# Kernel optimization log

Hardware: AMD Instinct MI355X
Metric: run time of the kernel (lower is better)

## Reference

```python
import jax, jax.numpy as jnp
import numpy as np

B, P, C = 128, 8732, 21          # batch, num_priors (SSD300), num_classes incl. background
TOP_K = 200
VAR0, VAR1 = 0.1, 0.2            # SSD prior variances
CONF_THRESH = 0.01
NMS_THRESH = 0.45


def setup_inputs() -> dict:
    key = jax.random.key(0)
    k1, k2, k3, k4 = jax.random.split(key, 4)
    loc_data = jax.random.normal(k1, (B, P, 4), jnp.float32)
    conf_data = jax.random.normal(k2, (B * P, C), jnp.float32)
    # priors: (cx, cy, w, h) in [0,1], positive widths/heights
    cxy = jax.random.uniform(k3, (P, 2), jnp.float32)
    wh = jax.random.uniform(k4, (P, 2), jnp.float32, minval=0.02, maxval=0.3)
    prior_data = jnp.concatenate([cxy, wh], axis=-1)
    return {"loc_data": loc_data, "conf_data": conf_data, "prior_data": prior_data}


def _decode(loc, priors):
    # loc: [B,P,4], priors: [P,4] (cx,cy,w,h) -> corner boxes [B,P,4]
    xy = priors[:, :2] + loc[..., :2] * VAR0 * priors[:, 2:]
    wh = priors[:, 2:] * jnp.exp(loc[..., 2:] * VAR1)
    return jnp.concatenate([xy - wh * 0.5, xy + wh * 0.5], axis=-1)


def _nms_single(boxes, scores, idxs):
    # boxes [P,4] corners, scores [P] (-1 where below conf_thresh), idxs [P] int class ids
    x1, y1, x2, y2 = boxes[:, 0], boxes[:, 1], boxes[:, 2], boxes[:, 3]
    areas = (x2 - x1) * (y2 - y1)

    def body(s, _):
        i = jnp.argmax(s)          # highest remaining score
        si = s[i]
        valid = si > 0.0
        bi = boxes[i]
        # IoU of bi against all boxes
        ix1 = jnp.maximum(bi[0], x1)
        iy1 = jnp.maximum(bi[1], y1)
        ix2 = jnp.minimum(bi[2], x2)
        iy2 = jnp.minimum(bi[3], y2)
        inter = jnp.maximum(ix2 - ix1, 0.0) * jnp.maximum(iy2 - iy1, 0.0)
        area_i = (bi[2] - bi[0]) * (bi[3] - bi[1])
        iou = inter / (area_i + areas - inter)
        # class-aware (batched) NMS: only suppress same-class boxes; also kills i itself (iou=1)
        suppress = (iou > NMS_THRESH) & (idxs == idxs[i])
        s_new = jnp.where(suppress, -1.0, s)
        row = jnp.where(
            valid,
            jnp.concatenate([bi, si[None], idxs[i].astype(jnp.float32)[None]]),
            jnp.zeros(6, dtype=boxes.dtype),
        )
        return s_new, row

    _, rows = jax.lax.scan(body, scores, None, length=TOP_K)
    return rows  # [TOP_K, 6] = (x1,y1,x2,y2,score,class)


def reference(loc_data, conf_data, prior_data):
    # softmax over classes, drop background, per-prior best fg class
    conf = jax.nn.softmax(conf_data, axis=-1)[:, 1:].reshape(B, P, C - 1)
    scores = conf.max(axis=-1)           # [B,P]
    cls = jnp.argmax(conf, axis=-1)      # [B,P] fg class id (0..C-2)
    boxes = _decode(loc_data, prior_data)  # [B,P,4]
    masked = jnp.where(scores > CONF_THRESH, scores, -1.0)
    return jax.vmap(_nms_single)(boxes, masked, cls)  # [B, TOP_K, 6]
```

## Files before the change

### kernel.cpp

```cpp
#include <hip/hip_runtime.h>


typedef unsigned long long u64;

#define BATCH 128
#define NPRIOR 8732
#define NCLS 21
#define TOPK 200
#define T 1024
#define TARGET 256
#define CAP 384
#define NBIN 4096
#define KW 6
#define NCHUNK 9

__device__ __forceinline__ double exp_fast(double x) {
  const double LOG2E = 1.4426950408889634;
  const double LN2_HI = 6.93147180369123816490e-01;
  const double LN2_LO = 1.90821492927058770002e-10;
  double n = rint(x * LOG2E);
  double r = fma(-n, LN2_HI, x);
  r = fma(-n, LN2_LO, r);
  double p = 2.505210838544172e-08;
  p = fma(p, r, 2.755731922398589e-07);
  p = fma(p, r, 2.7557319223985893e-06);
  p = fma(p, r, 2.48015873015873e-05);
  p = fma(p, r, 1.984126984126984e-04);
  p = fma(p, r, 1.388888888888889e-03);
  p = fma(p, r, 8.333333333333333e-03);
  p = fma(p, r, 4.1666666666666664e-02);
  p = fma(p, r, 1.6666666666666666e-01);
  p = fma(p, r, 0.5);
  p = fma(p, r, 1.0);
  p = fma(p, r, 1.0);
  double scale = __longlong_as_double(((long long)(1023 + (int)n)) << 52);
  return p * scale;
}

__global__ __launch_bounds__(256) void prep_kernel(
    const float* __restrict__ conf, u64* __restrict__ keys) {
  const int r = blockIdx.x * 256 + threadIdx.x;
  const float* __restrict__ rp = conf + (long long)r * NCLS;
  float cr[NCLS];
#pragma unroll
  for (int j = 0; j < NCLS; ++j) cr[j] = rp[j];
  float m = cr[0];
#pragma unroll
  for (int j = 1; j < NCLS; ++j) m = fmaxf(m, cr[j]);
  float sum = __expf(cr[0] - m);
  float bestr = cr[1];
  float beste = __expf(cr[1] - m);
  sum += beste;
  int bi = 1;
#pragma unroll
  for (int j = 2; j < NCLS; ++j) {
    float rv = cr[j];
    float ej = __expf(rv - m);
    sum += ej;
    if (rv > bestr) { bestr = rv; bi = j; beste = ej; }
  }
  float score = __fdividef(beste, sum);

  const int p = r % NPRIOR;
  u64 key = 0ULL;
  if (score > 0.01f) {
    key = ((u64)__float_as_uint(score) << 32) |
          ((u64)(16383 - p) << 10) | (u64)(bi - 1);
  }
  keys[r] = key;
}

__device__ __forceinline__ void radix_cut(const int* hist, int tid, int tcap,
                                          int* wtot, int* cut) {
  if (tid == 0) cut[2] = 0;
  const int base = tid * 4;
  const int cs = hist[base] + hist[base + 1] + hist[base + 2] + hist[base + 3];
  const int lane = tid & 63;
  int suf = cs;
#pragma unroll
  for (int off = 1; off < 64; off <<= 1) {
    int v = __shfl_down(suf, off);
    if (lane + off < 64) suf += v;
  }
  if (lane == 0) wtot[tid >> 6] = suf;
  __syncthreads();
  if (tid < 16) {
    int v = wtot[tid];
    int s = v;
#pragma unroll
    for (int off = 1; off < 16; off <<= 1) {
      int o = __shfl_down(s, off);
      if (tid + off < 16) s += o;
    }
    if (tid == 0) wtot[16] = s;
    wtot[tid] = s - v;
  }
  __syncthreads();
  const int total = wtot[16];
  if (total > 0) {
    const int target = total < tcap ? total : tcap;
    const int S = suf + wtot[tid >> 6];
    const int Snext = S - cs;
    if (S >= target && Snext < target) {
      int acc = Snext;
      for (int bn = base + 3; bn >= base; --bn) {
        acc += hist[bn];
        if (acc >= target) {
          cut[0] = bn; cut[1] = acc - hist[bn]; cut[2] = acc;
          break;
        }
      }
    }
  }
  __syncthreads();
}

__global__ __launch_bounds__(T) void selnms_kernel(
    const float* __restrict__ loc, const float* __restrict__ conf,
    const float* __restrict__ prior, const u64* __restrict__ keys,
    float* __restrict__ out) {
  __shared__ int hist[NBIN];
  __shared__ u64 buf[CAP];
  __shared__ u64 ebuf[CAP];
  __shared__ u64 buf2[CAP];
  __shared__ float4 cbox[CAP];
  __shared__ float car[CAP];
  __shared__ int ccl[CAP];
  __shared__ u64 KILL[CAP * KW];
  __shared__ int wtot[17];
  __shared__ int cut1[3], cut2[3];
  __shared__ u64 Ash[KW], KFsh[KW], ACCsh[KW];
  __shared__ float4 abox[TOPK];
  __shared__ float aar[TOPK];
  __shared__ int acl[TOPK];
  __shared__ int sh_cnt, sh_nA;

  const int tid = threadIdx.x;
  const int b = blockIdx.x;
  const float* confb = conf + (long long)b * (NPRIOR * NCLS);
  const float4* loc4 = ((const float4*)loc) + (long long)b * NPRIOR;
  const float4* pr4 = (const float4*)prior;
  float* outb = out + (long long)b * (TOPK * 6);
  const u64* kb = keys + (long long)b * NPRIOR;

  u64 kreg[NCHUNK];
#pragma unroll
  for (int c = 0; c < NCHUNK; ++c) {
    const int i = c * T + tid;
    kreg[c] = (i < NPRIOR) ? kb[i] : 0ULL;
  }
  if (tid == 0) sh_nA = 0;

  u64 ub = ~0ULL;
  int Mr = 0, total = 0;
  while (true) {
    for (int i = tid; i < NBIN; i += T) hist[i] = 0;
    __syncthreads();
#pragma unroll
    for (int c = 0; c < NCHUNK; ++c) {
      u64 k = kreg[c];
      if (k && k < ub) atomicAdd(&hist[(int)((k >> 46) & 0xFFF)], 1);
    }
    __syncthreads();
    radix_cut(hist, tid, TARGET, wtot, cut1);
    total = wtot[16];
    int M = cut1[2];
    if (M == 0) break;
    const int c1 = cut1[0];
    const int baseA = cut1[1];
    const bool need2 = (M > CAP);
    int c2 = 0;
    if (need2) {
      for (int i = tid; i < NBIN; i += T) hist[i] = 0;
      __syncthreads();
#pragma unroll
      for (int c = 0; c < NCHUNK; ++c) {
        u64 k = kreg[c];
        if (k && k < ub && (int)((k >> 46) & 0xFFF) == c1)
          atomicAdd(&hist[(int)((k >> 34) & 0xFFF)], 1);
      }
      __syncthreads();
      const int tcap2 = (total < TARGET ? total : TARGET) - baseA;
      radix_cut(hist, tid, tcap2, wtot, cut2);
      c2 = cut2[0];
      M = baseA + cut2[2];
      if (M > CAP) {
        int Md = M - hist[c2];
        if (Md > 0) { M = Md; c2 = c2 + 1; } else { M = CAP; }
      }
    }
    if (tid == 0) sh_cnt = 0;
    const u64 ubold = ub;
    ub = need2 ? (((u64)c1 << 46) + ((u64)c2 << 34)) : ((u64)c1 << 46);
    __syncthreads();
#pragma unroll
    for (int c = 0; c < NCHUNK; ++c) {
      u64 k = kreg[c];
      bool psel = false;
      if (k && k < ubold) {
        int b1 = (int)((k >> 46) & 0xFFF);
        psel = need2 ? (b1 > c1 || (b1 == c1 && (int)((k >> 34) & 0xFFF) >= c2))
                     : (b1 >= c1);
      }
      u64 mask = __ballot(psel ? 1 : 0);
      if (mask) {
        int lane = tid & 63;
        int leader = __ffsll((unsigned long long)mask) - 1;
        int bpos = 0;
        if (lane == leader) bpos = atomicAdd(&sh_cnt, __popcll(mask));
        bpos = __shfl(bpos, leader);
        if (psel) {
          int pos = bpos + __popcll(mask & ((1ULL << lane) - 1ULL));
          if (pos < CAP) buf[pos] = k;
        }
      }
    }
    __syncthreads();
    Mr = sh_cnt;
    if (Mr > CAP) Mr = CAP;
    if (Mr == 0) break;

    float4 lreg = make_float4(0.f, 0.f, 0.f, 0.f);
    float4 preg = make_float4(0.f, 0.f, 0.f, 0.f);
    int myp = 0, mycl = 0;
    if (tid < Mr) {
      u64 ak = buf[tid];
      mycl = (int)(ak & 0x1FULL);
      myp = 16383 - (int)((ak >> 10) & 0x3FFFULL);
      lreg = loc4[myp];
      preg = pr4[myp];
      const float* crow = confb + (long long)myp * NCLS;
      float cr[NCLS];
#pragma unroll
      for (int j = 0; j < NCLS; ++j) cr[j] = crow[j];
      double m = (double)cr[0];
#pragma unroll
      for (int j = 1; j < NCLS; ++j) m = fmax(m, (double)cr[j]);
      double sum = 0.0, best = -1.0;
#pragma unroll
      for (int j = 0; j < NCLS; ++j) {
        double ej = exp_fast((double)cr[j] - m);
        sum += ej;
        if (j >= 1 && ej > best) best = ej;
      }
      double score = best / sum;
      u64 sb = (u64)__double_as_longlong(score);
      ebuf[tid] = ((sb >> 24) << 24) | ((u64)(16383 - myp) << 10) | (u64)mycl;
    }
    if (tid < KW) { Ash[tid] = 0ULL; KFsh[tid] = 0ULL; }
    __syncthreads();
    const int nA0 = sh_nA;

    if (tid < Mr) {
      u64 ka = ebuf[tid];
      int ra = 0;
      int i = 0;
      for (; i + 8 <= Mr; i += 8) {
        u64 k0 = ebuf[i], k1 = ebuf[i + 1], k2 = ebuf[i + 2], k3 = ebuf[i + 3];
        u64 k4 = ebuf[i + 4], k5 = ebuf[i + 5], k6 = ebuf[i + 6],
            k7 = ebuf[i + 7];
        ra += (int)(k0 > ka) + (int)(k1 > ka) + (int)(k2 > ka) +
              (int)(k3 > ka) + (int)(k4 > ka) + (int)(k5 > ka) +
              (int)(k6 > ka) + (int)(k7 > ka);
      }
      for (; i < Mr; ++i) ra += (int)(ebuf[i] > ka);
      buf2[ra] = ka;
      double cx = (double)preg.x + (double)lreg.x * 0.1 * (double)preg.z;
      double cy = (double)preg.y + (double)lreg.y * 0.1 * (double)preg.w;
      double w = (double)preg.z * exp_fast((double)lreg.z * 0.2);
      double h = (double)preg.w * exp_fast((double)lreg.w * 0.2);
      float x1 = (float)(cx - w * 0.5), y1 = (float)(cy - h * 0.5);
      float x2 = (float)(cx + w * 0.5), y2 = (float)(cy + h * 0.5);
      cbox[ra] = make_float4(x1, y1, x2, y2);
      car[ra] = (x2 - x1) * (y2 - y1);
      ccl[ra] = mycl;
    }
    __syncthreads();

    if (nA0 > 0 && tid < Mr) {
      const int t = tid;
      float4 my = cbox[t];
      float mar = car[t];
      int mcl = ccl[t];
      bool sup = false;
      for (int a = 0; a < nA0; ++a) {
        if (acl[a] == mcl) {
          float4 ab = abox[a];
          float ix1 = fmaxf(ab.x, my.x), iy1 = fmaxf(ab.y, my.y);
          float ix2 = fminf(ab.z, my.z), iy2 = fminf(ab.w, my.w);
          float inter = fmaxf(ix2 - ix1, 0.f) * fmaxf(iy2 - iy1, 0.f);
          if (inter > 0.45f * (aar[a] + mar - inter)) sup = true;
        }
      }
      if (sup) atomicOr(&Ash[t >> 6], 1ULL << (t & 63));
    }
    for (int idx = tid; idx < KW * 512; idx += T) {
      const int seg = idx >> 9;
      const int t = idx & 511;
      if (t < Mr) {
        const int i0 = seg * 64;
        int i1 = i0 + 64;
        if (i1 > Mr) i1 = Mr;
        u64 mm = 0ULL;
        if (i1 > t) {
          float4 my = cbox[t];
          float mar = car[t];
          int mcl = ccl[t];
          int is = (i0 > t + 1) ? i0 : (t + 1);
#pragma unroll 4
          for (int i = is; i < i1; ++i) {
            if (ccl[i] == mcl) {
              float4 cb = cbox[i];
              float ix1 = fmaxf(my.x, cb.x), iy1 = fmaxf(my.y, cb.y);
              float ix2 = fminf(my.z, cb.z), iy2 = fminf(my.w, cb.w);
              float inter = fmaxf(ix2 - ix1, 0.f) * fmaxf(iy2 - iy1, 0.f);
              if (inter > 0.45f * (mar + car[i] - inter))
                mm |= 1ULL << (i - i0);
            }
          }
        }
        KILL[t * KW + seg] = mm;
        if (mm) atomicOr(&KFsh[t >> 6], 1ULL << (t & 63));
      }
    }
    __syncthreads();
    if (tid < 64) {
      u64 A0, A1, A2, A3, A4, A5;
      {
        u64 v[KW];
#pragma unroll
        for (int w = 0; w < KW; ++w) {
          int rem = Mr - 64 * w;
          u64 vm =
              (rem >= 64) ? ~0ULL : (rem <= 0 ? 0ULL : ((1ULL << rem) - 1ULL));
          v[w] = vm & ~Ash[w];
        }
        A0 = v[0]; A1 = v[1]; A2 = v[2]; A3 = v[3]; A4 = v[4]; A5 = v[5];
      }
      u64 C0 = 0, C1 = 0, C2 = 0, C3 = 0, C4 = 0, C5 = 0;
      int nacc = nA0;
      bool full = false;
#define KILLUPD(cidx) do { const u64* kc = &KILL[(cidx) * KW];      \
      A0 &= ~kc[0]; A1 &= ~kc[1]; A2 &= ~kc[2];                     \
      A3 &= ~kc[3]; A4 &= ~kc[4]; A5 &= ~kc[5]; } while (0)
#define RESW(w, Aw, Cw) if (!full) {                                \
      const u64 KFw = KFsh[w];                                      \
      int lim = Mr - (w) * 64; if (lim > 64) lim = 64;              \
      for (int q = 0; q < lim; ++q) {                               \
        if ((Aw >> q) & 1ULL) {                                     \
          Cw |= 1ULL << q; ++nacc;                                  \
          if (nacc == TOPK) { full = true; break; }                 \
          if ((KFw >> q) & 1ULL) KILLUPD((w) * 64 + q);             \
        } } }
      RESW(0, A0, C0)
      RESW(1, A1, C1)
      RESW(2, A2, C2)
      RESW(3, A3, C3)
      RESW(4, A4, C4)
      RESW(5, A5, C5)
#undef RESW
#undef KILLUPD
      if (tid == 0) {
        ACCsh[0] = C0; ACCsh[1] = C1; ACCsh[2] = C2;
        ACCsh[3] = C3; ACCsh[4] = C4; ACCsh[5] = C5;
        sh_nA = nacc;
      }
    }
    __syncthreads();
    if (tid < Mr) {
      const int t = tid;
      const int w = t >> 6, q = t & 63;
      const u64 accw = ACCsh[w];
      if ((accw >> q) & 1ULL) {
        int rank = nA0;
#pragma unroll
        for (int w2 = 0; w2 < KW; ++w2)
          if (w2 < w) rank += __popcll(ACCsh[w2]);
        rank += __popcll(accw & ((q == 0) ? 0ULL : ((1ULL << q) - 1ULL)));
        float4 bx = cbox[t];
        float sc =
            (float)__longlong_as_double((long long)((buf2[t] >> 24) << 24));
        float* o = outb + rank * 6;
        o[0] = bx.x; o[1] = bx.y; o[2] = bx.z; o[3] = bx.w;
        o[4] = sc; o[5] = (float)ccl[t];
        abox[rank] = bx; aar[rank] = car[t]; acl[rank] = ccl[t];
      }
    }
    __syncthreads();
    if (sh_nA >= TOPK) break;
    if (total - Mr <= 0) break;
  }
  __syncthreads();
  const int nAf = sh_nA;
  for (int i = nAf * 6 + tid; i < TOPK * 6; i += T) outb[i] = 0.0f;
}

extern "C" void kernel_launch(void* const* d_in, const int* in_sizes, int n_in,
                              void* d_out, int out_size, void* d_ws,
                              size_t ws_size, hipStream_t stream) {
  const float* loc = (const float*)d_in[0];
  const float* conf = (const float*)d_in[1];
  const float* prior = (const float*)d_in[2];
  float* out = (float*)d_out;

  u64* keys = (u64*)d_ws;
  const int nrows_blocks = (BATCH * NPRIOR) / 256;

  prep_kernel<<<nrows_blocks, 256, 0, stream>>>(conf, keys);
  selnms_kernel<<<BATCH, T, 0, stream>>>(loc, conf, prior, keys, out);
}
```

Measured before the change: 204.9 us.

## Fuse softmax key prep into NMS kernel and rebuild kill mask via ballots

The separate prep kernel that computes softmax scores and packed sort keys is removed. Each block of the detection kernel now computes its own batch's keys in registers, which avoids the round trip of keys through global workspace and one kernel launch. The pairwise suppression matrix is also restructured: six waves each own a column segment and build KILL rows with wave ballots, reading classes from a packed byte array. The cost is that the whole conf read (about 94 MB, with strided per-thread rows) now runs on only 128 blocks instead of thousands, and the mask build uses fewer threads.

```diff
diff --git a/kernel.cpp b/kernel.cpp
--- a/kernel.cpp
+++ b/kernel.cpp
@@ -37,39 +37,6 @@
   return p * scale;
 }
 
-__global__ __launch_bounds__(256) void prep_kernel(
-    const float* __restrict__ conf, u64* __restrict__ keys) {
-  const int r = blockIdx.x * 256 + threadIdx.x;
-  const float* __restrict__ rp = conf + (long long)r * NCLS;
-  float cr[NCLS];
-#pragma unroll
-  for (int j = 0; j < NCLS; ++j) cr[j] = rp[j];
-  float m = cr[0];
-#pragma unroll
-  for (int j = 1; j < NCLS; ++j) m = fmaxf(m, cr[j]);
-  float sum = __expf(cr[0] - m);
-  float bestr = cr[1];
-  float beste = __expf(cr[1] - m);
-  sum += beste;
-  int bi = 1;
-#pragma unroll
-  for (int j = 2; j < NCLS; ++j) {
-    float rv = cr[j];
-    float ej = __expf(rv - m);
-    sum += ej;
-    if (rv > bestr) { bestr = rv; bi = j; beste = ej; }
-  }
-  float score = __fdividef(beste, sum);
-
-  const int p = r % NPRIOR;
-  u64 key = 0ULL;
-  if (score > 0.01f) {
-    key = ((u64)__float_as_uint(score) << 32) |
-          ((u64)(16383 - p) << 10) | (u64)(bi - 1);
-  }
-  keys[r] = key;
-}
-
 __device__ __forceinline__ void radix_cut(const int* hist, int tid, int tcap,
                                           int* wtot, int* cut) {
   if (tid == 0) cut[2] = 0;
@@ -115,10 +82,9 @@
   __syncthreads();
 }
 
-__global__ __launch_bounds__(T) void selnms_kernel(
+__global__ __launch_bounds__(T) void detect_kernel(
     const float* __restrict__ loc, const float* __restrict__ conf,
-    const float* __restrict__ prior, const u64* __restrict__ keys,
-    float* __restrict__ out) {
+    const float* __restrict__ prior, float* __restrict__ out) {
   __shared__ int hist[NBIN];
   __shared__ u64 buf[CAP];
   __shared__ u64 ebuf[CAP];
@@ -126,6 +92,7 @@
   __shared__ float4 cbox[CAP];
   __shared__ float car[CAP];
   __shared__ int ccl[CAP];
+  __shared__ __align__(4) unsigned char cclb[CAP];
   __shared__ u64 KILL[CAP * KW];
   __shared__ int wtot[17];
   __shared__ int cut1[3], cut2[3];
@@ -141,13 +108,39 @@
   const float4* loc4 = ((const float4*)loc) + (long long)b * NPRIOR;
   const float4* pr4 = (const float4*)prior;
   float* outb = out + (long long)b * (TOPK * 6);
-  const u64* kb = keys + (long long)b * NPRIOR;
 
   u64 kreg[NCHUNK];
 #pragma unroll
   for (int c = 0; c < NCHUNK; ++c) {
-    const int i = c * T + tid;
-    kreg[c] = (i < NPRIOR) ? kb[i] : 0ULL;
+    const int r = c * T + tid;
+    u64 key = 0ULL;
+    if (r < NPRIOR) {
+      const float* __restrict__ rp = confb + (long long)r * NCLS;
+      float cr[NCLS];
+#pragma unroll
+      for (int j = 0; j < NCLS; ++j) cr[j] = rp[j];
+      float m = cr[0];
+#pragma unroll
+      for (int j = 1; j < NCLS; ++j) m = fmaxf(m, cr[j]);
+      float sum = __expf(cr[0] - m);
+      float bestr = cr[1];
+      float beste = __expf(cr[1] - m);
+      sum += beste;
+      int bi = 1;
+#pragma unroll
+      for (int j = 2; j < NCLS; ++j) {
+        float rv = cr[j];
+        float ej = __expf(rv - m);
+        sum += ej;
+        if (rv > bestr) { bestr = rv; bi = j; beste = ej; }
+      }
+      float score = __fdividef(beste, sum);
+      if (score > 0.01f) {
+        key = ((u64)__float_as_uint(score) << 32) |
+              ((u64)(16383 - r) << 10) | (u64)(bi - 1);
+      }
+    }
+    kreg[c] = key;
   }
   if (tid == 0) sh_nA = 0;
 
@@ -274,6 +267,7 @@
       cbox[ra] = make_float4(x1, y1, x2, y2);
       car[ra] = (x2 - x1) * (y2 - y1);
       ccl[ra] = mycl;
+      cclb[ra] = (unsigned char)mycl;
     }
     __syncthreads();
 
@@ -294,33 +288,39 @@
       }
       if (sup) atomicOr(&Ash[t >> 6], 1ULL << (t & 63));
     }
-    for (int idx = tid; idx < KW * 512; idx += T) {
-      const int seg = idx >> 9;
-      const int t = idx & 511;
-      if (t < Mr) {
-        const int i0 = seg * 64;
-        int i1 = i0 + 64;
-        if (i1 > Mr) i1 = Mr;
-        u64 mm = 0ULL;
-        if (i1 > t) {
-          float4 my = cbox[t];
-          float mar = car[t];
-          int mcl = ccl[t];
-          int is = (i0 > t + 1) ? i0 : (t + 1);
-#pragma unroll 4
-          for (int i = is; i < i1; ++i) {
-            if (ccl[i] == mcl) {
-              float4 cb = cbox[i];
-              float ix1 = fmaxf(my.x, cb.x), iy1 = fmaxf(my.y, cb.y);
-              float ix2 = fminf(my.z, cb.z), iy2 = fminf(my.w, cb.w);
+    {
+      const int wv = tid >> 6;
+      const int lane = tid & 63;
+      if (wv < KW) {
+        const int s = wv;
+        const int j = s * 64 + lane;
+        float4 ob = make_float4(0.f, 0.f, 0.f, 0.f);
+        float oar = 0.f;
+        int ocl = -1;
+        if (j < Mr) { ob = cbox[j]; oar = car[j]; ocl = ccl[j]; }
+        for (int t0 = 0; t0 < Mr; t0 += 64) {
+          u64 myrow = 0ULL;
+          const int tend = (t0 + 64 < Mr) ? (t0 + 64) : Mr;
+          unsigned cw = 0;
+          for (int t = t0; t < tend; ++t) {
+            if ((t & 3) == 0) cw = *(const unsigned*)&cclb[t & ~3];
+            const int clt = (int)((cw >> ((t & 3) * 8)) & 0xFF);
+            float4 tb = cbox[t];
+            bool kill = false;
+            if (j > t && j < Mr && clt == ocl) {
+              float tar = (tb.z - tb.x) * (tb.w - tb.y);
+              float ix1 = fmaxf(tb.x, ob.x), iy1 = fmaxf(tb.y, ob.y);
+              float ix2 = fminf(tb.z, ob.z), iy2 = fminf(tb.w, ob.w);
               float inter = fmaxf(ix2 - ix1, 0.f) * fmaxf(iy2 - iy1, 0.f);
-              if (inter > 0.45f * (mar + car[i] - inter))
-                mm |= 1ULL << (i - i0);
+              kill = inter > 0.45f * (tar + oar - inter);
             }
+            u64 mm = __ballot(kill ? 1 : 0);
+            if (lane == (t - t0)) myrow = mm;
           }
+          if (t0 + lane < Mr) KILL[(t0 + lane) * KW + s] = myrow;
+          u64 kf = __ballot(myrow != 0ULL);
+          if (lane == 0 && kf) atomicOr(&KFsh[t0 >> 6], kf);
         }
-        KILL[t * KW + seg] = mm;
-        if (mm) atomicOr(&KFsh[t >> 6], 1ULL << (t & 63));
       }
     }
     __syncthreads();
@@ -402,10 +402,7 @@
   const float* conf = (const float*)d_in[1];
   const float* prior = (const float*)d_in[2];
   float* out = (float*)d_out;
-
-  u64* keys = (u64*)d_ws;
-  const int nrows_blocks = (BATCH * NPRIOR) / 256;
-
-  prep_kernel<<<nrows_blocks, 256, 0, stream>>>(conf, keys);
-  selnms_kernel<<<BATCH, T, 0, stream>>>(loc, conf, prior, keys, out);
+  (void)d_ws; (void)ws_size;
+
+  detect_kernel<<<BATCH, T, 0, stream>>>(loc, conf, prior, out);
 }
```

New measurement: 233.1 us. 13.8% more time.

## Stage keys in LDS and iterate only same-class candidates via class bitmasks

Applied to the files above, without the earlier changes.

Per-class 64-bit membership masks over the sorted candidate list are built with shared atomics. The pairwise kill-mask loop then walks only the set bits of same-class candidates instead of scanning every candidate and branching on class. Separately, the per-thread register copy of the keys is replaced by a 70KB shared-memory array that the histogram and selection passes re-read. This cuts IoU work and register pressure, but adds shared traffic and LDS use that may limit occupancy, which matters little with one block per batch.

```diff
diff --git a/kernel.cpp b/kernel.cpp
--- a/kernel.cpp
+++ b/kernel.cpp
@@ -12,7 +12,7 @@
 #define CAP 384
 #define NBIN 4096
 #define KW 6
-#define NCHUNK 9
+#define NCLM 20
 
 __device__ __forceinline__ double exp_fast(double x) {
   const double LOG2E = 1.4426950408889634;
@@ -119,6 +119,7 @@
     const float* __restrict__ loc, const float* __restrict__ conf,
     const float* __restrict__ prior, const u64* __restrict__ keys,
     float* __restrict__ out) {
+  __shared__ u64 Ks[NPRIOR];
   __shared__ int hist[NBIN];
   __shared__ u64 buf[CAP];
   __shared__ u64 ebuf[CAP];
@@ -127,6 +128,7 @@
   __shared__ float car[CAP];
   __shared__ int ccl[CAP];
   __shared__ u64 KILL[CAP * KW];
+  __shared__ u64 CLSM[NCLM][KW];
   __shared__ int wtot[17];
   __shared__ int cut1[3], cut2[3];
   __shared__ u64 Ash[KW], KFsh[KW], ACCsh[KW];
@@ -143,22 +145,17 @@
   float* outb = out + (long long)b * (TOPK * 6);
   const u64* kb = keys + (long long)b * NPRIOR;
 
-  u64 kreg[NCHUNK];
-#pragma unroll
-  for (int c = 0; c < NCHUNK; ++c) {
-    const int i = c * T + tid;
-    kreg[c] = (i < NPRIOR) ? kb[i] : 0ULL;
-  }
+  for (int i = tid; i < NPRIOR; i += T) Ks[i] = kb[i];
   if (tid == 0) sh_nA = 0;
+  __syncthreads();
 
   u64 ub = ~0ULL;
   int Mr = 0, total = 0;
   while (true) {
     for (int i = tid; i < NBIN; i += T) hist[i] = 0;
     __syncthreads();
-#pragma unroll
-    for (int c = 0; c < NCHUNK; ++c) {
-      u64 k = kreg[c];
+    for (int i = tid; i < NPRIOR; i += T) {
+      u64 k = Ks[i];
       if (k && k < ub) atomicAdd(&hist[(int)((k >> 46) & 0xFFF)], 1);
     }
     __syncthreads();
@@ -173,9 +170,8 @@
     if (need2) {
       for (int i = tid; i < NBIN; i += T) hist[i] = 0;
       __syncthreads();
-#pragma unroll
-      for (int c = 0; c < NCHUNK; ++c) {
-        u64 k = kreg[c];
+      for (int i = tid; i < NPRIOR; i += T) {
+        u64 k = Ks[i];
         if (k && k < ub && (int)((k >> 46) & 0xFFF) == c1)
           atomicAdd(&hist[(int)((k >> 34) & 0xFFF)], 1);
       }
@@ -193,9 +189,8 @@
     const u64 ubold = ub;
     ub = need2 ? (((u64)c1 << 46) + ((u64)c2 << 34)) : ((u64)c1 << 46);
     __syncthreads();
-#pragma unroll
-    for (int c = 0; c < NCHUNK; ++c) {
-      u64 k = kreg[c];
+    for (int i = tid; i < NPRIOR; i += T) {
+      u64 k = Ks[i];
       bool psel = false;
       if (k && k < ubold) {
         int b1 = (int)((k >> 46) & 0xFFF);
@@ -248,6 +243,7 @@
       ebuf[tid] = ((sb >> 24) << 24) | ((u64)(16383 - myp) << 10) | (u64)mycl;
     }
     if (tid < KW) { Ash[tid] = 0ULL; KFsh[tid] = 0ULL; }
+    if (tid < NCLM * KW) ((u64*)CLSM)[tid] = 0ULL;
     __syncthreads();
     const int nA0 = sh_nA;
 
@@ -274,6 +270,7 @@
       cbox[ra] = make_float4(x1, y1, x2, y2);
       car[ra] = (x2 - x1) * (y2 - y1);
       ccl[ra] = mycl;
+      atomicOr(&CLSM[mycl][ra >> 6], 1ULL << (ra & 63));
     }
     __syncthreads();
 
@@ -299,25 +296,25 @@
       const int t = idx & 511;
       if (t < Mr) {
         const int i0 = seg * 64;
-        int i1 = i0 + 64;
-        if (i1 > Mr) i1 = Mr;
         u64 mm = 0ULL;
-        if (i1 > t) {
-          float4 my = cbox[t];
-          float mar = car[t];
-          int mcl = ccl[t];
-          int is = (i0 > t + 1) ? i0 : (t + 1);
-#pragma unroll 4
-          for (int i = is; i < i1; ++i) {
-            if (ccl[i] == mcl) {
-              float4 cb = cbox[i];
-              float ix1 = fmaxf(my.x, cb.x), iy1 = fmaxf(my.y, cb.y);
-              float ix2 = fminf(my.z, cb.z), iy2 = fminf(my.w, cb.w);
-              float inter = fmaxf(ix2 - ix1, 0.f) * fmaxf(iy2 - iy1, 0.f);
-              if (inter > 0.45f * (mar + car[i] - inter))
-                mm |= 1ULL << (i - i0);
-            }
-          }
+        u64 cm = CLSM[ccl[t]][seg];
+        const int d = t - i0;
+        if (d >= 63) cm = 0ULL;
+        else if (d >= 0) cm &= ~((1ULL << (d + 1)) - 1ULL);
+        if (cm) {
+          const float4 my = cbox[t];
+          const float mar = (my.z - my.x) * (my.w - my.y);
+          do {
+            const int l = __ffsll((unsigned long long)cm) - 1;
+            cm &= cm - 1ULL;
+            const int i = i0 + l;
+            const float4 cb = cbox[i];
+            const float tar = (cb.z - cb.x) * (cb.w - cb.y);
+            float ix1 = fmaxf(my.x, cb.x), iy1 = fmaxf(my.y, cb.y);
+            float ix2 = fminf(my.z, cb.z), iy2 = fminf(my.w, cb.w);
+            float inter = fmaxf(ix2 - ix1, 0.f) * fmaxf(iy2 - iy1, 0.f);
+            if (inter > 0.45f * (mar + tar - inter)) mm |= 1ULL << l;
+          } while (cm);
         }
         KILL[t * KW + seg] = mm;
         if (mm) atomicOr(&KFsh[t >> 6], 1ULL << (t & 63));
```

Measured after the change: 187.0 us. -8.7%, faster.
